# Optimization experiments

Hardware: AMD Instinct MI355X
Metric: run time of the kernel (lower is better)

## Reference

```python
import jax, jax.numpy as jnp
import numpy as np

B, S, H, L, D, DI = 4, 32, 8, 128, 512, 2048
EPS = 1e-6
TEMP = float(D) ** 0.5


def layer_norm(x, g, b):
    mu = jnp.mean(x, axis=-1, keepdims=True)
    var = jnp.mean((x - mu) ** 2, axis=-1, keepdims=True)
    return (x - mu) * jax.lax.rsqrt(var + EPS) * g + b


def setup_inputs() -> dict:
    key = jax.random.key(0)
    ks = jax.random.split(key, 8)
    x = jax.random.normal(ks[0], (B, S, L, D), jnp.float32)
    mask = jax.random.randint(ks[1], (B, S, L), 0, 2, jnp.int32)
    # learned params
    w = jax.random.normal(ks[2], (1, 1, H, L, D), jnp.float32) * (1.0 / np.sqrt(D))
    v_w = jax.random.normal(ks[3], (D, D), jnp.float32) * 0.02   # nn.Linear weight (out,in)
    ln_g = jnp.ones((D,), jnp.float32)
    ln_b = jnp.zeros((D,), jnp.float32)
    w1 = jax.random.normal(ks[4], (DI, D), jnp.float32) * 0.02
    b1 = jnp.zeros((DI,), jnp.float32)
    w2 = jax.random.normal(ks[5], (D, DI), jnp.float32) * 0.02
    b2 = jnp.zeros((D,), jnp.float32)
    fln_g = jnp.ones((D,), jnp.float32)
    fln_b = jnp.zeros((D,), jnp.float32)
    return {"x": x, "mask": mask, "w": w, "v_w": v_w, "ln_g": ln_g, "ln_b": ln_b,
            "w1": w1, "b1": b1, "w2": w2, "b2": b2, "fln_g": fln_g, "fln_b": fln_b}


def reference(x, mask, w, v_w, ln_g, ln_b, w1, b1, w2, b2, fln_g, fln_b):
    # attn logits: broadcast mul + reduce over d_model == einsum over d
    attn = jnp.einsum('bsld,hld->bshl', x, w[0, 0]) / TEMP           # (B,S,H,L)
    attn = jnp.where(mask[:, :, None, :] == 0, -1e9, attn)
    attn = jax.nn.softmax(attn, axis=-1)                              # dropout: eval mode
    v = jnp.einsum('bsld,ed->bsle', x, v_w)                           # Linear no bias: x @ W.T
    out = jnp.einsum('bsld,bshl->bshd', v, attn)                      # weighted sum readout
    out = layer_norm(out, ln_g, ln_b)
    # PositionwiseFeedForward with residual + LayerNorm
    h = jax.nn.relu(jnp.einsum('bshd,fd->bshf', out, w1) + b1)
    y = jnp.einsum('bshf,df->bshd', h, w2) + b2 + out
    y = layer_norm(y, fln_g, fln_b)
    return y, attn
```

## Files before the change

kernel.cpp:

```cpp
#include <hip/hip_runtime.h>
#include <hip/hip_bf16.h>

#define BB 4
#define SS 32
#define HH 8
#define LL 128
#define DD 512
#define DI 2048
#define EPSN 1e-6f
#define INV_TEMP 0.04419417382415922f

#define NLOGIT_BLK 4096
#define NCAST_GRAN ((DI*DD/4)*2 + (DD*DD/4))
#define NCAST_BLK (NCAST_GRAN / 256)

#define NROW (BB*SS*HH)
#define SLICE ((size_t)NROW * DD)

typedef __attribute__((ext_vector_type(8))) short short8;
typedef __attribute__((ext_vector_type(4))) float float4v;

static __device__ __forceinline__ unsigned short f2b(float f) {
  __hip_bfloat16 h = __float2bfloat16(f);
  return *(unsigned short*)&h;
}

__global__ __launch_bounds__(256) void pre_kernel(
    const float* __restrict__ x, const int* __restrict__ mask,
    const float* __restrict__ w, const float* __restrict__ w1,
    const float* __restrict__ w2, const float* __restrict__ v_w,
    unsigned short* __restrict__ w1b, unsigned short* __restrict__ w2b,
    unsigned short* __restrict__ v_wb, float* __restrict__ logits) {
  int blk = blockIdx.x;
  if (blk < NLOGIT_BLK) {
    int wv = threadIdx.x >> 6, lane = threadIdx.x & 63;
    int p  = blk * 4 + wv;
    int bs = p >> 7, l = p & (LL - 1);

    const float4* xr = (const float4*)(x + ((size_t)bs * LL + l) * DD) + lane * 2;
    float4 x0 = xr[0], x1 = xr[1];

    float acc[HH];
#pragma unroll
    for (int h = 0; h < HH; ++h) {
      const float4* wr = (const float4*)(w + ((size_t)h * LL + l) * DD) + lane * 2;
      float4 w0 = wr[0], w1v = wr[1];
      acc[h] = x0.x * w0.x + x0.y * w0.y + x0.z * w0.z + x0.w * w0.w +
               x1.x * w1v.x + x1.y * w1v.y + x1.z * w1v.z + x1.w * w1v.w;
    }
#pragma unroll
    for (int off = 32; off > 0; off >>= 1) {
#pragma unroll
      for (int h = 0; h < HH; ++h) acc[h] += __shfl_xor(acc[h], off);
    }
    if (lane == 0) {
      int msk = mask[bs * LL + l];
#pragma unroll
      for (int h = 0; h < HH; ++h) {
        float lg = msk ? acc[h] * INV_TEMP : -1e9f;
        logits[((size_t)bs * HH + h) * LL + l] = lg;
      }
    }
  } else {
    const int n1 = (DI * DD) / 4;
    const int n2 = n1;
    int i = (blk - NLOGIT_BLK) * 256 + threadIdx.x;
    const float4* src;
    unsigned short* dst;
    int j = i;
    if (i < n1)           { src = (const float4*)w1;  dst = w1b; }
    else if (i < n1 + n2) { src = (const float4*)w2;  dst = w2b;  j = i - n1; }
    else                  { src = (const float4*)v_w; dst = v_wb; j = i - n1 - n2; }
    float4 v = src[j];
    dst[j * 4 + 0] = f2b(v.x);
    dst[j * 4 + 1] = f2b(v.y);
    dst[j * 4 + 2] = f2b(v.z);
    dst[j * 4 + 3] = f2b(v.w);
  }
}

__global__ __launch_bounds__(512) void xa_kernel(
    const float* __restrict__ x, const float* __restrict__ logits,
    float* __restrict__ attn_out, unsigned short* __restrict__ xab) {
  int bs = blockIdx.x >> 1, half = blockIdx.x & 1;
  int t = threadIdx.x, wv = t >> 6, lane = t & 63;

  __shared__ float sattn_t[LL][HH];
  __shared__ float sxa[2][HH][256];

  if (wv < 4) {
    for (int h = wv; h < HH; h += 4) {
      const float* lg = logits + ((size_t)bs * HH + h) * LL;
      float v0 = lg[lane], v1 = lg[lane + 64];
      float m = fmaxf(v0, v1);
#pragma unroll
      for (int off = 32; off > 0; off >>= 1) m = fmaxf(m, __shfl_xor(m, off));
      float e0 = __expf(v0 - m), e1 = __expf(v1 - m);
      float s = e0 + e1;
#pragma unroll
      for (int off = 32; off > 0; off >>= 1) s += __shfl_xor(s, off);
      float inv = 1.f / s;
      e0 *= inv; e1 *= inv;
      sattn_t[lane][h]      = e0;
      sattn_t[lane + 64][h] = e1;
      if (half == 0) {
        float* ao = attn_out + ((size_t)bs * HH + h) * LL;
        ao[lane]      = e0;
        ao[lane + 64] = e1;
      }
    }
  }
  __syncthreads();

  int col = t & 255, lseg = t >> 8;
  int e = half * 256 + col;
  const float* xb = x + (size_t)bs * LL * DD;
  float acc[HH];
#pragma unroll
  for (int h = 0; h < HH; ++h) acc[h] = 0.f;
  int l0 = lseg * 64;
  for (int l = l0; l < l0 + 64; ++l) {
    float xv = xb[(size_t)l * DD + e];
    float4 a0 = *(const float4*)&sattn_t[l][0];
    float4 a1 = *(const float4*)&sattn_t[l][4];
    acc[0] += a0.x * xv; acc[1] += a0.y * xv;
    acc[2] += a0.z * xv; acc[3] += a0.w * xv;
    acc[4] += a1.x * xv; acc[5] += a1.y * xv;
    acc[6] += a1.z * xv; acc[7] += a1.w * xv;
  }
#pragma unroll
  for (int h = 0; h < HH; ++h) sxa[lseg][h][col] = acc[h];
  __syncthreads();
  if (t < 256) {
    unsigned short* xo = xab + (size_t)bs * HH * DD;
#pragma unroll
    for (int h = 0; h < HH; ++h)
      xo[h * DD + t + half * 256] = f2b(sxa[0][h][t] + sxa[1][h][t]);
  }
}

__global__ __launch_bounds__(256) void gemm_v_kernel(
    const unsigned short* __restrict__ xab, const unsigned short* __restrict__ v_wb,
    float* __restrict__ vpart) {
  int blk = blockIdx.x;
  int nt = blk & 7, mt = (blk >> 3) & 15, kslice = blk >> 7;
  int wv = threadIdx.x >> 6, lane = threadIdx.x & 63;
  int lm = lane & 15, lq = lane >> 4;

  int m0 = mt * 64 + wv * 16;
  int n0 = nt * 64;
  int g0 = kslice * 16;

  const short8* A0 = (const short8*)(xab + (size_t)(m0 + lm) * DD) + g0;
  const short8* Bp[4];
#pragma unroll
  for (int nf = 0; nf < 4; ++nf)
    Bp[nf] = (const short8*)(v_wb + (size_t)(n0 + nf * 16 + lm) * DD) + g0;

  float4v acc[4];
#pragma unroll
  for (int nf = 0; nf < 4; ++nf) acc[nf] = (float4v){0.f, 0.f, 0.f, 0.f};

#pragma unroll
  for (int ks = 0; ks < 4; ++ks) {
    short8 a0 = A0[ks * 4 + lq];
    short8 b[4];
#pragma unroll
    for (int nf = 0; nf < 4; ++nf) b[nf] = Bp[nf][ks * 4 + lq];
#pragma unroll
    for (int nf = 0; nf < 4; ++nf)
      acc[nf] = __builtin_amdgcn_mfma_f32_16x16x32_bf16(a0, b[nf], acc[nf], 0, 0, 0);
  }

  float* outp = vpart + (size_t)kslice * SLICE;
#pragma unroll
  for (int nf = 0; nf < 4; ++nf) {
    int col = n0 + nf * 16 + lm;
#pragma unroll
    for (int r = 0; r < 4; ++r) {
      int row = m0 + lq * 4 + r;
      outp[(size_t)row * DD + col] = acc[nf][r];
    }
  }
}

__global__ __launch_bounds__(256) void ln_mid_kernel(
    const float* __restrict__ vpart, const float* __restrict__ ln_g,
    const float* __restrict__ ln_b, float* __restrict__ o_ln,
    unsigned short* __restrict__ o_lnb) {
  int wv = threadIdx.x >> 6, lane = threadIdx.x & 63;
  int row = blockIdx.x * 4 + wv;

  const float* p0 = vpart + (size_t)row * DD;
  float vals[8];
  float sum = 0.f, sq = 0.f;
#pragma unroll
  for (int k = 0; k < 8; ++k) {
    int d = lane + 64 * k;
    float v = p0[d] + p0[SLICE + d] + p0[2 * SLICE + d] + p0[3 * SLICE + d];
    vals[k] = v;
    sum += v;
    sq += v * v;
  }
#pragma unroll
  for (int off = 32; off > 0; off >>= 1) {
    sum += __shfl_xor(sum, off);
    sq  += __shfl_xor(sq, off);
  }
  float mu  = sum * (1.f / DD);
  float var = sq * (1.f / DD) - mu * mu;
  float rs  = rsqrtf(var + EPSN);
  float* op = o_ln + (size_t)row * DD;
  unsigned short* opb = o_lnb + (size_t)row * DD;
#pragma unroll
  for (int k = 0; k < 8; ++k) {
    int d = lane + 64 * k;
    float v = (vals[k] - mu) * rs * ln_g[d] + ln_b[d];
    op[d]  = v;
    opb[d] = f2b(v);
  }
}

__global__ __launch_bounds__(256) void gemm1_kernel(
    const unsigned short* __restrict__ xb, const unsigned short* __restrict__ w1b,
    const float* __restrict__ b1, unsigned short* __restrict__ h1b) {
  int blk = blockIdx.x;
  int nt = blk & 31, mt = blk >> 5;
  int wv = threadIdx.x >> 6, lane = threadIdx.x & 63;
  int lm = lane & 15, lq = lane >> 4;

  int m0 = mt * 64 + wv * 16;
  int n0 = nt * 64;

  const short8* A0 = (const short8*)(xb + (size_t)(m0 + lm) * DD);
  const short8* Bp[4];
#pragma unroll
  for (int nf = 0; nf < 4; ++nf)
    Bp[nf] = (const short8*)(w1b + (size_t)(n0 + nf * 16 + lm) * DD);

  float4v acc[4];
#pragma unroll
  for (int nf = 0; nf < 4; ++nf) acc[nf] = (float4v){0.f, 0.f, 0.f, 0.f};

#pragma unroll 4
  for (int ks = 0; ks < DD / 32; ++ks) {
    short8 a0 = A0[ks * 4 + lq];
    short8 b[4];
#pragma unroll
    for (int nf = 0; nf < 4; ++nf) b[nf] = Bp[nf][ks * 4 + lq];
#pragma unroll
    for (int nf = 0; nf < 4; ++nf)
      acc[nf] = __builtin_amdgcn_mfma_f32_16x16x32_bf16(a0, b[nf], acc[nf], 0, 0, 0);
  }

#pragma unroll
  for (int nf = 0; nf < 4; ++nf) {
    int col = n0 + nf * 16 + lm;
    float bb = b1[col];
#pragma unroll
    for (int r = 0; r < 4; ++r) {
      int row = m0 + lq * 4 + r;
      float v = acc[nf][r] + bb;
      h1b[(size_t)row * DI + col] = f2b(fmaxf(v, 0.f));
    }
  }
}

__global__ __launch_bounds__(256) void gemm2_kernel(
    const unsigned short* __restrict__ h1b, const unsigned short* __restrict__ w2b,
    float* __restrict__ ypart) {
  int blk = blockIdx.x;
  int nt = blk & 7, mt = (blk >> 3) & 15, kslice = blk >> 7;
  int wv = threadIdx.x >> 6, lane = threadIdx.x & 63;
  int lm = lane & 15, lq = lane >> 4;

  int m0 = mt * 64 + wv * 16;
  int n0 = nt * 64;
  int g0 = kslice * 64;

  const short8* A0 = (const short8*)(h1b + (size_t)(m0 + lm) * DI) + g0;
  const short8* Bp[4];
#pragma unroll
  for (int nf = 0; nf < 4; ++nf)
    Bp[nf] = (const short8*)(w2b + (size_t)(n0 + nf * 16 + lm) * DI) + g0;

  float4v acc[4];
#pragma unroll
  for (int nf = 0; nf < 4; ++nf) acc[nf] = (float4v){0.f, 0.f, 0.f, 0.f};

#pragma unroll 4
  for (int ks = 0; ks < 16; ++ks) {
    short8 a0 = A0[ks * 4 + lq];
    short8 b[4];
#pragma unroll
    for (int nf = 0; nf < 4; ++nf) b[nf] = Bp[nf][ks * 4 + lq];
#pragma unroll
    for (int nf = 0; nf < 4; ++nf)
      acc[nf] = __builtin_amdgcn_mfma_f32_16x16x32_bf16(a0, b[nf], acc[nf], 0, 0, 0);
  }

  float* outp = ypart + (size_t)kslice * SLICE;
#pragma unroll
  for (int nf = 0; nf < 4; ++nf) {
    int col = n0 + nf * 16 + lm;
#pragma unroll
    for (int r = 0; r < 4; ++r) {
      int row = m0 + lq * 4 + r;
      outp[(size_t)row * DD + col] = acc[nf][r];
    }
  }
}

__global__ __launch_bounds__(256) void ln_final_kernel(
    const float* __restrict__ ypart, const float* __restrict__ o_ln,
    const float* __restrict__ b2, const float* __restrict__ fln_g,
    const float* __restrict__ fln_b, float* __restrict__ y_out) {
  int wv = threadIdx.x >> 6, lane = threadIdx.x & 63;
  int row = blockIdx.x * 4 + wv;

  const float* p0 = ypart + (size_t)row * DD;
  const float* ol = o_ln + (size_t)row * DD;
  float vals[8];
  float sum = 0.f, sq = 0.f;
#pragma unroll
  for (int k = 0; k < 8; ++k) {
    int d = lane + 64 * k;
    float v = p0[d] + p0[SLICE + d] + p0[2 * SLICE + d] + p0[3 * SLICE + d] +
              b2[d] + ol[d];
    vals[k] = v;
    sum += v;
    sq += v * v;
  }
#pragma unroll
  for (int off = 32; off > 0; off >>= 1) {
    sum += __shfl_xor(sum, off);
    sq  += __shfl_xor(sq, off);
  }
  float mu  = sum * (1.f / DD);
  float var = sq * (1.f / DD) - mu * mu;
  float rs  = rsqrtf(var + EPSN);
  float* yo = y_out + (size_t)row * DD;
#pragma unroll
  for (int k = 0; k < 8; ++k) {
    int d = lane + 64 * k;
    yo[d] = (vals[k] - mu) * rs * fln_g[d] + fln_b[d];
  }
}

extern "C" void kernel_launch(void* const* d_in, const int* in_sizes, int n_in,
                              void* d_out, int out_size, void* d_ws, size_t ws_size,
                              hipStream_t stream) {
  const float* x     = (const float*)d_in[0];
  const int*   mask  = (const int*)d_in[1];
  const float* w     = (const float*)d_in[2];
  const float* v_w   = (const float*)d_in[3];
  const float* ln_g  = (const float*)d_in[4];
  const float* ln_b  = (const float*)d_in[5];
  const float* w1    = (const float*)d_in[6];
  const float* b1    = (const float*)d_in[7];
  const float* w2    = (const float*)d_in[8];
  const float* b2    = (const float*)d_in[9];
  const float* fln_g = (const float*)d_in[10];
  const float* fln_b = (const float*)d_in[11];

  float* y    = (float*)d_out;
  float* attn = y + (size_t)BB * SS * HH * DD;

  char* ws = (char*)d_ws;
  float*          o_ln    = (float*)(ws);
  unsigned short* o_lnb   = (unsigned short*)(ws + 2097152);
  unsigned short* w1b     = (unsigned short*)(ws + 3145728);
  unsigned short* w2b     = (unsigned short*)(ws + 5242880);
  unsigned short* h1b     = (unsigned short*)(ws + 7340032);
  float*          ypart   = (float*)(ws + 11534336);
  unsigned short* v_wb    = (unsigned short*)(ws + 19922944);
  unsigned short* xab     = (unsigned short*)(ws + 20447232);
  float*          vpart   = (float*)(ws + 21495808);
  float*          logits  = (float*)(ws + 29884416);

  pre_kernel<<<NLOGIT_BLK + NCAST_BLK, 256, 0, stream>>>(
      x, mask, w, w1, w2, v_w, w1b, w2b, v_wb, logits);
  xa_kernel<<<BB * SS * 2, 512, 0, stream>>>(x, logits, attn, xab);
  gemm_v_kernel<<<512, 256, 0, stream>>>(xab, v_wb, vpart);
  ln_mid_kernel<<<256, 256, 0, stream>>>(vpart, ln_g, ln_b, o_ln, o_lnb);
  gemm1_kernel<<<512, 256, 0, stream>>>(o_lnb, w1b, b1, h1b);
  gemm2_kernel<<<512, 256, 0, stream>>>(h1b, w2b, ypart);
  ln_final_kernel<<<256, 256, 0, stream>>>(ypart, o_ln, b2, fln_g, fln_b, y);
}
```

Before: 172.6 us.

## Store bf16 GEMM operands in MFMA fragment-packed layout for coalesced loads

```diff
diff --git a/kernel.cpp b/kernel.cpp
--- a/kernel.cpp
+++ b/kernel.cpp
@@ -23,6 +23,11 @@
 static __device__ __forceinline__ unsigned short f2b(float f) {
   __hip_bfloat16 h = __float2bfloat16(f);
   return *(unsigned short*)&h;
+}
+
+static __device__ __forceinline__ size_t pk(int m, int k, int K) {
+  return ((((size_t)(m >> 4) * (K >> 5) + (k >> 5)) * 4 + ((k >> 3) & 3)) * 16
+          + (m & 15)) * 8 + (k & 7);
 }
 
 __global__ __launch_bounds__(256) void pre_kernel(
@@ -65,17 +70,28 @@
     const int n1 = (DI * DD) / 4;
     const int n2 = n1;
     int i = (blk - NLOGIT_BLK) * 256 + threadIdx.x;
-    const float4* src;
+    float4 v;
     unsigned short* dst;
-    int j = i;
-    if (i < n1)           { src = (const float4*)w1;  dst = w1b; }
-    else if (i < n1 + n2) { src = (const float4*)w2;  dst = w2b;  j = i - n1; }
-    else                  { src = (const float4*)v_w; dst = v_wb; j = i - n1 - n2; }
-    float4 v = src[j];
-    dst[j * 4 + 0] = f2b(v.x);
-    dst[j * 4 + 1] = f2b(v.y);
-    dst[j * 4 + 2] = f2b(v.z);
-    dst[j * 4 + 3] = f2b(v.w);
+    size_t base;
+    if (i < n1) {
+      v = ((const float4*)w1)[i];
+      dst = w1b;
+      base = pk(i >> 7, (i & 127) * 4, DD);
+    } else if (i < n1 + n2) {
+      int j = i - n1;
+      v = ((const float4*)w2)[j];
+      dst = w2b;
+      base = pk(j >> 9, (j & 511) * 4, DI);
+    } else {
+      int j = i - n1 - n2;
+      v = ((const float4*)v_w)[j];
+      dst = v_wb;
+      base = pk(j >> 7, (j & 127) * 4, DD);
+    }
+    dst[base + 0] = f2b(v.x);
+    dst[base + 1] = f2b(v.y);
+    dst[base + 2] = f2b(v.z);
+    dst[base + 3] = f2b(v.w);
   }
 }
 
@@ -132,10 +148,11 @@
   for (int h = 0; h < HH; ++h) sxa[lseg][h][col] = acc[h];
   __syncthreads();
   if (t < 256) {
-    unsigned short* xo = xab + (size_t)bs * HH * DD;
-#pragma unroll
-    for (int h = 0; h < HH; ++h)
-      xo[h * DD + t + half * 256] = f2b(sxa[0][h][t] + sxa[1][h][t]);
+#pragma unroll
+    for (int h = 0; h < HH; ++h) {
+      int m = bs * HH + h;
+      xab[pk(m, e, DD)] = f2b(sxa[0][h][t] + sxa[1][h][t]);
+    }
   }
 }
 
@@ -149,27 +166,22 @@
 
   int m0 = mt * 64 + wv * 16;
   int n0 = nt * 64;
-  int g0 = kslice * 16;
-
-  const short8* A0 = (const short8*)(xab + (size_t)(m0 + lm) * DD) + g0;
-  const short8* Bp[4];
-#pragma unroll
-  for (int nf = 0; nf < 4; ++nf)
-    Bp[nf] = (const short8*)(v_wb + (size_t)(n0 + nf * 16 + lm) * DD) + g0;
+  const short8* A8 = (const short8*)xab + (size_t)(m0 >> 4) * 16 * 64;
+  const short8* B8 = (const short8*)v_wb;
 
   float4v acc[4];
 #pragma unroll
   for (int nf = 0; nf < 4; ++nf) acc[nf] = (float4v){0.f, 0.f, 0.f, 0.f};
 
 #pragma unroll
-  for (int ks = 0; ks < 4; ++ks) {
-    short8 a0 = A0[ks * 4 + lq];
-    short8 b[4];
-#pragma unroll
-    for (int nf = 0; nf < 4; ++nf) b[nf] = Bp[nf][ks * 4 + lq];
-#pragma unroll
-    for (int nf = 0; nf < 4; ++nf)
-      acc[nf] = __builtin_amdgcn_mfma_f32_16x16x32_bf16(a0, b[nf], acc[nf], 0, 0, 0);
+  for (int ci = 0; ci < 4; ++ci) {
+    int c = kslice * 4 + ci;
+    short8 a = A8[(size_t)c * 64 + lane];
+#pragma unroll
+    for (int nf = 0; nf < 4; ++nf) {
+      short8 b = B8[((size_t)((n0 >> 4) + nf) * 16 + c) * 64 + lane];
+      acc[nf] = __builtin_amdgcn_mfma_f32_16x16x32_bf16(a, b, acc[nf], 0, 0, 0);
+    }
   }
 
   float* outp = vpart + (size_t)kslice * SLICE;
@@ -177,10 +189,8 @@
   for (int nf = 0; nf < 4; ++nf) {
     int col = n0 + nf * 16 + lm;
 #pragma unroll
-    for (int r = 0; r < 4; ++r) {
-      int row = m0 + lq * 4 + r;
-      outp[(size_t)row * DD + col] = acc[nf][r];
-    }
+    for (int r = 0; r < 4; ++r)
+      outp[(size_t)(m0 + lq * 4 + r) * DD + col] = acc[nf][r];
   }
 }
 
@@ -211,18 +221,17 @@
   float var = sq * (1.f / DD) - mu * mu;
   float rs  = rsqrtf(var + EPSN);
   float* op = o_ln + (size_t)row * DD;
-  unsigned short* opb = o_lnb + (size_t)row * DD;
 #pragma unroll
   for (int k = 0; k < 8; ++k) {
     int d = lane + 64 * k;
     float v = (vals[k] - mu) * rs * ln_g[d] + ln_b[d];
-    op[d]  = v;
-    opb[d] = f2b(v);
+    op[d] = v;
+    o_lnb[pk(row, d, DD)] = f2b(v);
   }
 }
 
 __global__ __launch_bounds__(256) void gemm1_kernel(
-    const unsigned short* __restrict__ xb, const unsigned short* __restrict__ w1b,
+    const unsigned short* __restrict__ o_lnb, const unsigned short* __restrict__ w1b,
     const float* __restrict__ b1, unsigned short* __restrict__ h1b) {
   int blk = blockIdx.x;
   int nt = blk & 31, mt = blk >> 5;
@@ -231,26 +240,21 @@
 
   int m0 = mt * 64 + wv * 16;
   int n0 = nt * 64;
-
-  const short8* A0 = (const short8*)(xb + (size_t)(m0 + lm) * DD);
-  const short8* Bp[4];
-#pragma unroll
-  for (int nf = 0; nf < 4; ++nf)
-    Bp[nf] = (const short8*)(w1b + (size_t)(n0 + nf * 16 + lm) * DD);
+  const short8* A8 = (const short8*)o_lnb + (size_t)(m0 >> 4) * 16 * 64;
+  const short8* B8 = (const short8*)w1b;
 
   float4v acc[4];
 #pragma unroll
   for (int nf = 0; nf < 4; ++nf) acc[nf] = (float4v){0.f, 0.f, 0.f, 0.f};
 
 #pragma unroll 4
-  for (int ks = 0; ks < DD / 32; ++ks) {
-    short8 a0 = A0[ks * 4 + lq];
-    short8 b[4];
-#pragma unroll
-    for (int nf = 0; nf < 4; ++nf) b[nf] = Bp[nf][ks * 4 + lq];
-#pragma unroll
-    for (int nf = 0; nf < 4; ++nf)
-      acc[nf] = __builtin_amdgcn_mfma_f32_16x16x32_bf16(a0, b[nf], acc[nf], 0, 0, 0);
+  for (int c = 0; c < 16; ++c) {
+    short8 a = A8[(size_t)c * 64 + lane];
+#pragma unroll
+    for (int nf = 0; nf < 4; ++nf) {
+      short8 b = B8[((size_t)((n0 >> 4) + nf) * 16 + c) * 64 + lane];
+      acc[nf] = __builtin_amdgcn_mfma_f32_16x16x32_bf16(a, b, acc[nf], 0, 0, 0);
+    }
   }
 
 #pragma unroll
@@ -260,8 +264,7 @@
 #pragma unroll
     for (int r = 0; r < 4; ++r) {
       int row = m0 + lq * 4 + r;
-      float v = acc[nf][r] + bb;
-      h1b[(size_t)row * DI + col] = f2b(fmaxf(v, 0.f));
+      h1b[pk(row, col, DI)] = f2b(fmaxf(acc[nf][r] + bb, 0.f));
     }
   }
 }
@@ -276,27 +279,22 @@
 
   int m0 = mt * 64 + wv * 16;
   int n0 = nt * 64;
-  int g0 = kslice * 64;
-
-  const short8* A0 = (const short8*)(h1b + (size_t)(m0 + lm) * DI) + g0;
-  const short8* Bp[4];
-#pragma unroll
-  for (int nf = 0; nf < 4; ++nf)
-    Bp[nf] = (const short8*)(w2b + (size_t)(n0 + nf * 16 + lm) * DI) + g0;
+  const short8* A8 = (const short8*)h1b + (size_t)(m0 >> 4) * 64 * 64;
+  const short8* B8 = (const short8*)w2b;
 
   float4v acc[4];
 #pragma unroll
   for (int nf = 0; nf < 4; ++nf) acc[nf] = (float4v){0.f, 0.f, 0.f, 0.f};
 
 #pragma unroll 4
-  for (int ks = 0; ks < 16; ++ks) {
-    short8 a0 = A0[ks * 4 + lq];
-    short8 b[4];
-#pragma unroll
-    for (int nf = 0; nf < 4; ++nf) b[nf] = Bp[nf][ks * 4 + lq];
-#pragma unroll
-    for (int nf = 0; nf < 4; ++nf)
-      acc[nf] = __builtin_amdgcn_mfma_f32_16x16x32_bf16(a0, b[nf], acc[nf], 0, 0, 0);
+  for (int ci = 0; ci < 16; ++ci) {
+    int c = kslice * 16 + ci;
+    short8 a = A8[(size_t)c * 64 + lane];
+#pragma unroll
+    for (int nf = 0; nf < 4; ++nf) {
+      short8 b = B8[((size_t)((n0 >> 4) + nf) * 64 + c) * 64 + lane];
+      acc[nf] = __builtin_amdgcn_mfma_f32_16x16x32_bf16(a, b, acc[nf], 0, 0, 0);
+    }
   }
 
   float* outp = ypart + (size_t)kslice * SLICE;
@@ -304,10 +302,8 @@
   for (int nf = 0; nf < 4; ++nf) {
     int col = n0 + nf * 16 + lm;
 #pragma unroll
-    for (int r = 0; r < 4; ++r) {
-      int row = m0 + lq * 4 + r;
-      outp[(size_t)row * DD + col] = acc[nf][r];
-    }
+    for (int r = 0; r < 4; ++r)
+      outp[(size_t)(m0 + lq * 4 + r) * DD + col] = acc[nf][r];
   }
 }
 
@@ -367,16 +363,16 @@
   float* attn = y + (size_t)BB * SS * HH * DD;
 
   char* ws = (char*)d_ws;
-  float*          o_ln    = (float*)(ws);
-  unsigned short* o_lnb   = (unsigned short*)(ws + 2097152);
-  unsigned short* w1b     = (unsigned short*)(ws + 3145728);
-  unsigned short* w2b     = (unsigned short*)(ws + 5242880);
-  unsigned short* h1b     = (unsigned short*)(ws + 7340032);
-  float*          ypart   = (float*)(ws + 11534336);
-  unsigned short* v_wb    = (unsigned short*)(ws + 19922944);
-  unsigned short* xab     = (unsigned short*)(ws + 20447232);
-  float*          vpart   = (float*)(ws + 21495808);
-  float*          logits  = (float*)(ws + 29884416);
+  float*          o_ln   = (float*)(ws);
+  unsigned short* o_lnb  = (unsigned short*)(ws + 2097152);
+  unsigned short* w1b    = (unsigned short*)(ws + 3145728);
+  unsigned short* w2b    = (unsigned short*)(ws + 5242880);
+  unsigned short* h1b    = (unsigned short*)(ws + 7340032);
+  float*          ypart  = (float*)(ws + 11534336);
+  unsigned short* v_wb   = (unsigned short*)(ws + 19922944);
+  unsigned short* xab    = (unsigned short*)(ws + 20447232);
+  float*          vpart  = (float*)(ws + 21495808);
+  float*          logits = (float*)(ws + 29884416);
 
   pre_kernel<<<NLOGIT_BLK + NCAST_BLK, 256, 0, stream>>>(
       x, mask, w, w1, w2, v_w, w1b, w2b, v_wb, logits);
```

Measured after the change: 155.1 us. 1.11x faster.
